# Kernel optimization log

Measured on AMD Instinct MI355X. Metric: run time of the kernel, lower is better.

Reference implementation:

```python
import jax, jax.numpy as jnp
import numpy as np

N, E, D, H, L = 50000, 800000, 64, 4, 2
DH = D // H


def layer_norm(h, g, b, eps=1e-5):
    mu = h.mean(-1, keepdims=True)
    var = ((h - mu) ** 2).mean(-1, keepdims=True)
    return (h - mu) / jnp.sqrt(var + eps) * g + b


def setup_inputs() -> dict:
    key = jax.random.key(0)
    ks = jax.random.split(key, 16)
    s = 1.0 / np.sqrt(D)
    inp = {
        "x": jax.random.normal(ks[0], (N, D), jnp.float32),
        "edge_attr": jax.random.normal(ks[1], (E, D), jnp.float32),
        "edge_index": jax.random.randint(ks[2], (2, E), 0, N, jnp.int64),
        "WQ": jax.random.normal(ks[3], (L, D, D), jnp.float32) * s,
        "WK": jax.random.normal(ks[4], (L, D, D), jnp.float32) * s,
        "WE": jax.random.normal(ks[5], (L, D, D), jnp.float32) * s,
        "WV": jax.random.normal(ks[6], (L, D, D), jnp.float32) * s,
        "WO": jax.random.normal(ks[7], (L, D, D), jnp.float32) * s,
        "bO": jnp.zeros((L, D), jnp.float32),
        "ln1_g": jnp.ones((L, D), jnp.float32),
        "ln1_b": jnp.zeros((L, D), jnp.float32),
        "W1": jax.random.normal(ks[8], (L, D, 2 * D), jnp.float32) * s,
        "b1": jnp.zeros((L, 2 * D), jnp.float32),
        "W2": jax.random.normal(ks[9], (L, 2 * D, D), jnp.float32) * (1.0 / np.sqrt(2 * D)),
        "b2": jnp.zeros((L, D), jnp.float32),
        "ln2_g": jnp.ones((L, D), jnp.float32),
        "ln2_b": jnp.zeros((L, D), jnp.float32),
    }
    return inp


def exphormer_layer(h, edge_attr, src, dst, p):
    (wq, wk, we, wv, wo, bo, g1, be1, w1, b1, w2, b2, g2, be2) = p
    n = h.shape[0]
    Qh = (h @ wq).reshape(n, H, DH)
    Kh = (h @ wk).reshape(n, H, DH)
    Vh = (h @ wv).reshape(n, H, DH)
    Eh = (edge_attr @ we).reshape(-1, H, DH)
    # per-edge score: sum over head_dim of K[src]*Q[dst]*E / sqrt(DH)
    s = jnp.sum(Kh[src] * Qh[dst] * Eh, axis=-1, keepdims=True) / np.sqrt(DH)
    score = jnp.exp(jnp.clip(s, -5.0, 5.0))  # [E, H, 1]
    msg = Vh[src] * score                     # [E, H, DH]
    wV = jax.ops.segment_sum(msg, dst, num_segments=n)    # [N, H, DH]
    Z = jax.ops.segment_sum(score, dst, num_segments=n)   # [N, H, 1]
    h_attn = (wV / (Z + 1e-6)).reshape(n, D)
    h1 = layer_norm(h + (h_attn @ wo + bo), g1, be1)
    ffn = jax.nn.relu(h1 @ w1 + b1) @ w2 + b2
    return layer_norm(h1 + ffn, g2, be2)


def reference(x, edge_attr, edge_index, WQ, WK, WE, WV, WO, bO, ln1_g, ln1_b,
              W1, b1, W2, b2, ln2_g, ln2_b):
    src = edge_index[0]
    dst = edge_index[1]
    h = x
    for l in range(L):
        p = (WQ[l], WK[l], WE[l], WV[l], WO[l], bO[l], ln1_g[l], ln1_b[l],
             W1[l], b1[l], W2[l], b2[l], ln2_g[l], ln2_b[l])
        h = exphormer_layer(h, edge_attr, src, dst, p)
    return h
```

## Files before the change

kernel.cpp:

```cpp
#include <hip/hip_runtime.h>

#define NN 50000
#define NE 800000
#define D  64
#define NL 2
#define NB 196

typedef __bf16 bf16x8 __attribute__((ext_vector_type(8)));
typedef float  floatx4 __attribute__((ext_vector_type(4)));

static __device__ __forceinline__ float bf2f(unsigned short u) {
    return __uint_as_float(((unsigned)u) << 16);
}
static __device__ __forceinline__ unsigned short f2bf(float x) {
    unsigned u = __float_as_uint(x);
    u += 0x7fff + ((u >> 16) & 1);
    return (unsigned short)(u >> 16);
}


__global__ void k_deg(const int* __restrict__ ei, int* __restrict__ deg) {
    int e = blockIdx.x * 256 + threadIdx.x;
    if (e < NE) atomicAdd(&deg[ei[NE + e]], 1);
}

__global__ __launch_bounds__(256) void k_scan1(const int* __restrict__ deg,
                                               int* __restrict__ psum) {
    __shared__ int red[4];
    int i = blockIdx.x * 256 + threadIdx.x;
    int v = (i < NN) ? deg[i] : 0;
#pragma unroll
    for (int m = 1; m < 64; m <<= 1) v += __shfl_xor(v, m, 64);
    if ((threadIdx.x & 63) == 0) red[threadIdx.x >> 6] = v;
    __syncthreads();
    if (threadIdx.x == 0) psum[blockIdx.x] = red[0] + red[1] + red[2] + red[3];
}

__global__ void k_scan2(int* __restrict__ psum) {
    __shared__ int buf[256];
    int t = threadIdx.x;
    int v = (t < NB) ? psum[t] : 0;
    buf[t] = v;
    __syncthreads();
    for (int o = 1; o < 256; o <<= 1) {
        int x = (t >= o) ? buf[t - o] : 0;
        __syncthreads();
        buf[t] += x;
        __syncthreads();
    }
    if (t < NB) psum[t] = buf[t] - v;
}

__global__ __launch_bounds__(256) void k_scan3(const int* __restrict__ deg,
                                               const int* __restrict__ psum,
                                               int* __restrict__ row_off,
                                               int* __restrict__ cursor) {
    __shared__ int buf[256];
    int t = threadIdx.x;
    int i = blockIdx.x * 256 + t;
    int v = (i < NN) ? deg[i] : 0;
    buf[t] = v;
    __syncthreads();
    for (int o = 1; o < 256; o <<= 1) {
        int x = (t >= o) ? buf[t - o] : 0;
        __syncthreads();
        buf[t] += x;
        __syncthreads();
    }
    if (i < NN) {
        int inc = buf[t] + psum[blockIdx.x];
        row_off[i + 1] = inc;
        cursor[i] = inc - v;
        if (i == 0) row_off[0] = 0;
    }
}

__global__ void k_scatter(const int* __restrict__ ei, int* __restrict__ cursor,
                          int* __restrict__ csr_src, int* __restrict__ eperm) {
    int e = blockIdx.x * 256 + threadIdx.x;
    if (e < NE) {
        int dst = ei[NE + e];
        int pos = atomicAdd(&cursor[dst], 1);
        csr_src[pos] = ei[e];
        eperm[e] = pos;
    }
}

__global__ __launch_bounds__(256) void k_prep(
        const float* __restrict__ WQ, const float* __restrict__ WK,
        const float* __restrict__ WV, const float* __restrict__ WE,
        const float* __restrict__ WO, const float* __restrict__ W1,
        const float* __restrict__ W2,
        unsigned short* __restrict__ wqT, unsigned short* __restrict__ wkT,
        unsigned short* __restrict__ wvT, unsigned short* __restrict__ weT,
        unsigned short* __restrict__ woT, unsigned short* __restrict__ w1T,
        unsigned short* __restrict__ w2T) {
    int idx = blockIdx.x * 256 + threadIdx.x;
    if (idx >= 2 * 36864) return;
    int l = idx / 36864;
    int r = idx % 36864;
    if (r < 20480) {
        int which = r >> 12, rr = r & 4095;
        int m = rr >> 6, k = rr & 63;
        const float* src = (which == 0 ? WQ : which == 1 ? WK : which == 2 ? WV :
                            which == 3 ? WE : WO);
        unsigned short* dst = (which == 0 ? wqT : which == 1 ? wkT : which == 2 ? wvT :
                               which == 3 ? weT : woT);
        dst[l * 4096 + rr] = f2bf(src[l * 4096 + k * 64 + m]);
    } else if (r < 28672) {
        int r2 = r - 20480;
        int m = r2 >> 6, k = r2 & 63;
        w1T[l * 8192 + r2] = f2bf(W1[l * 8192 + k * 128 + m]);
    } else {
        int r3 = r - 28672;
        int m = r3 >> 7, k = r3 & 127;
        w2T[l * 8192 + r3] = f2bf(W2[l * 8192 + k * 64 + m]);
    }
}


__global__ __launch_bounds__(256) void k_qkv_mfma(const float* __restrict__ h,
        const unsigned short* __restrict__ wqT, const unsigned short* __restrict__ wkT,
        const unsigned short* __restrict__ wvT,
        unsigned short* __restrict__ Qb, unsigned short* __restrict__ Kb,
        unsigned short* __restrict__ Vb) {
    __shared__ unsigned short st[4][16 * 72];
    const int lane = threadIdx.x & 63;
    const int w    = threadIdx.x >> 6;
    const int ml   = lane & 15;
    const int quad = lane >> 4;

    bf16x8 aq[2][4], ak[2][4], av[2][4];
#pragma unroll
    for (int kt = 0; kt < 2; kt++)
#pragma unroll
        for (int mt = 0; mt < 4; mt++) {
            int o = (mt*16 + ml)*64 + kt*32 + quad*8;
            aq[kt][mt] = *(const bf16x8*)&wqT[o];
            ak[kt][mt] = *(const bf16x8*)&wkT[o];
            av[kt][mt] = *(const bf16x8*)&wvT[o];
        }

    const int wave = blockIdx.x * 4 + w;
    const int nw   = gridDim.x * 4;
    const int el = lane >> 2, c = lane & 3;
    for (int tile = wave; tile < NN / 16; tile += nw) {
        const int e0 = tile * 16;
        const float4* ar = (const float4*)(h + (size_t)(e0 + ml) * D);
        bf16x8 b[2];
#pragma unroll
        for (int kt = 0; kt < 2; kt++) {
            float4 f0 = ar[kt*8 + quad*2 + 0];
            float4 f1 = ar[kt*8 + quad*2 + 1];
            b[kt][0] = (__bf16)f0.x; b[kt][1] = (__bf16)f0.y;
            b[kt][2] = (__bf16)f0.z; b[kt][3] = (__bf16)f0.w;
            b[kt][4] = (__bf16)f1.x; b[kt][5] = (__bf16)f1.y;
            b[kt][6] = (__bf16)f1.z; b[kt][7] = (__bf16)f1.w;
        }
        floatx4 accq[4] = {}, acck[4] = {}, accv[4] = {};
#pragma unroll
        for (int kt = 0; kt < 2; kt++)
#pragma unroll
            for (int mt = 0; mt < 4; mt++) {
                accq[mt] = __builtin_amdgcn_mfma_f32_16x16x32_bf16(aq[kt][mt], b[kt], accq[mt], 0, 0, 0);
                acck[mt] = __builtin_amdgcn_mfma_f32_16x16x32_bf16(ak[kt][mt], b[kt], acck[mt], 0, 0, 0);
                accv[mt] = __builtin_amdgcn_mfma_f32_16x16x32_bf16(av[kt][mt], b[kt], accv[mt], 0, 0, 0);
            }
#pragma unroll
        for (int mt = 0; mt < 4; mt++)
            *(ushort4*)&st[w][ml*72 + mt*16 + quad*4] =
                make_ushort4(f2bf(accq[mt][0]), f2bf(accq[mt][1]),
                             f2bf(accq[mt][2]), f2bf(accq[mt][3]));
        {
            uint4 r0 = *(const uint4*)&st[w][el*72 + c*16 + 0];
            uint4 r1 = *(const uint4*)&st[w][el*72 + c*16 + 8];
            uint4* gp = (uint4*)(Qb + (size_t)(e0 + el) * D + c*16);
            gp[0] = r0; gp[1] = r1;
        }
#pragma unroll
        for (int mt = 0; mt < 4; mt++)
            *(ushort4*)&st[w][ml*72 + mt*16 + quad*4] =
                make_ushort4(f2bf(acck[mt][0]), f2bf(acck[mt][1]),
                             f2bf(acck[mt][2]), f2bf(acck[mt][3]));
        {
            uint4 r0 = *(const uint4*)&st[w][el*72 + c*16 + 0];
            uint4 r1 = *(const uint4*)&st[w][el*72 + c*16 + 8];
            uint4* gp = (uint4*)(Kb + (size_t)(e0 + el) * D + c*16);
            gp[0] = r0; gp[1] = r1;
        }
#pragma unroll
        for (int mt = 0; mt < 4; mt++)
            *(ushort4*)&st[w][ml*72 + mt*16 + quad*4] =
                make_ushort4(f2bf(accv[mt][0]), f2bf(accv[mt][1]),
                             f2bf(accv[mt][2]), f2bf(accv[mt][3]));
        {
            uint4 r0 = *(const uint4*)&st[w][el*72 + c*16 + 0];
            uint4 r1 = *(const uint4*)&st[w][el*72 + c*16 + 8];
            uint4* gp = (uint4*)(Vb + (size_t)(e0 + el) * D + c*16);
            gp[0] = r0; gp[1] = r1;
        }
    }
}

__global__ __launch_bounds__(256) void k_eh_score(const float* __restrict__ ea,
        const unsigned short* __restrict__ weT, const int* __restrict__ eperm,
        const int* __restrict__ ei, const unsigned short* __restrict__ Qb,
        const unsigned short* __restrict__ Kb,
        float* __restrict__ scb, unsigned short* __restrict__ Eh1) {
    __shared__ unsigned short wsm[2 * 4608];
    __shared__ unsigned short st[4][16 * 72];
    const int t = threadIdx.x;
    for (int i = t; i < 1024; i += 256) {
        int l = i >> 9, r = i & 511;
        *(uint4*)&wsm[l*4608 + (r >> 3)*72 + (r & 7)*8] = ((const uint4*)weT)[i];
    }
    __syncthreads();

    const int lane = t & 63;
    const int w    = t >> 6;
    const int ml   = lane & 15;
    const int quad = lane >> 4;
    const int el = lane >> 2, c = lane & 3;
    const int wave = blockIdx.x * 4 + w;
    const int nw   = gridDim.x * 4;
    const int NT   = NE / 16;

    int tile = wave;
    if (tile >= NT) return;
    int srce = ei[tile*16 + el];
    int dste = ei[NE + tile*16 + el];
    int pose = eperm[tile*16 + el];
    const float4* ar0 = (const float4*)(ea + (size_t)(tile*16 + ml) * D);
    float4 f00 = ar0[quad*2 + 0];
    float4 f01 = ar0[quad*2 + 1];
    float4 f10 = ar0[8 + quad*2 + 0];
    float4 f11 = ar0[8 + quad*2 + 1];

    for (; tile < NT; tile += nw) {
        bf16x8 qg0 = *(const bf16x8*)(Qb + (size_t)dste * D + c*16);
        bf16x8 qg1 = *(const bf16x8*)(Qb + (size_t)dste * D + c*16 + 8);
        bf16x8 kg0 = *(const bf16x8*)(Kb + (size_t)srce * D + c*16);
        bf16x8 kg1 = *(const bf16x8*)(Kb + (size_t)srce * D + c*16 + 8);
        int nxt = tile + nw;
        float4 nf00 = f00, nf01 = f01, nf10 = f10, nf11 = f11;
        int nsrc = srce, ndst = dste, npos = pose;
        if (nxt < NT) {
            const float4* ar = (const float4*)(ea + (size_t)(nxt*16 + ml) * D);
            nf00 = ar[quad*2 + 0];
            nf01 = ar[quad*2 + 1];
            nf10 = ar[8 + quad*2 + 0];
            nf11 = ar[8 + quad*2 + 1];
            nsrc = ei[nxt*16 + el];
            ndst = ei[NE + nxt*16 + el];
            npos = eperm[nxt*16 + el];
        }
        bf16x8 b[2];
        b[0][0] = (__bf16)f00.x; b[0][1] = (__bf16)f00.y;
        b[0][2] = (__bf16)f00.z; b[0][3] = (__bf16)f00.w;
        b[0][4] = (__bf16)f01.x; b[0][5] = (__bf16)f01.y;
        b[0][6] = (__bf16)f01.z; b[0][7] = (__bf16)f01.w;
        b[1][0] = (__bf16)f10.x; b[1][1] = (__bf16)f10.y;
        b[1][2] = (__bf16)f10.z; b[1][3] = (__bf16)f10.w;
        b[1][4] = (__bf16)f11.x; b[1][5] = (__bf16)f11.y;
        b[1][6] = (__bf16)f11.z; b[1][7] = (__bf16)f11.w;

        {
            floatx4 acc[4] = {};
#pragma unroll
            for (int kt = 0; kt < 2; kt++)
#pragma unroll
                for (int mt = 0; mt < 4; mt++) {
                    bf16x8 a = *(const bf16x8*)&wsm[4608 + (mt*16 + ml)*72 + kt*32 + quad*8];
                    acc[mt] = __builtin_amdgcn_mfma_f32_16x16x32_bf16(a, b[kt], acc[mt], 0, 0, 0);
                }
#pragma unroll
            for (int mt = 0; mt < 4; mt++)
                *(ushort4*)&st[w][ml*72 + mt*16 + quad*4] =
                    make_ushort4(f2bf(acc[mt][0]), f2bf(acc[mt][1]),
                                 f2bf(acc[mt][2]), f2bf(acc[mt][3]));
            uint4 r0 = *(const uint4*)&st[w][el*72 + c*16 + 0];
            uint4 r1 = *(const uint4*)&st[w][el*72 + c*16 + 8];
            uint4* gp = (uint4*)(Eh1 + (size_t)(tile*16 + el) * D + c*16);
            gp[0] = r0;
            gp[1] = r1;
        }
        {
            floatx4 acc[4] = {};
#pragma unroll
            for (int kt = 0; kt < 2; kt++)
#pragma unroll
                for (int mt = 0; mt < 4; mt++) {
                    bf16x8 a = *(const bf16x8*)&wsm[(mt*16 + ml)*72 + kt*32 + quad*8];
                    acc[mt] = __builtin_amdgcn_mfma_f32_16x16x32_bf16(a, b[kt], acc[mt], 0, 0, 0);
                }
#pragma unroll
            for (int mt = 0; mt < 4; mt++)
                *(ushort4*)&st[w][ml*72 + mt*16 + quad*4] =
                    make_ushort4(f2bf(acc[mt][0]), f2bf(acc[mt][1]),
                                 f2bf(acc[mt][2]), f2bf(acc[mt][3]));
            bf16x8 e0v = *(const bf16x8*)&st[w][el*72 + c*16];
            bf16x8 e1v = *(const bf16x8*)&st[w][el*72 + c*16 + 8];
            float s = 0.f;
#pragma unroll
            for (int i = 0; i < 8; i++) s += (float)e0v[i] * (float)qg0[i] * (float)kg0[i];
#pragma unroll
            for (int i = 0; i < 8; i++) s += (float)e1v[i] * (float)qg1[i] * (float)kg1[i];
            scb[(size_t)pose * 4 + c] = __expf(fminf(5.f, fmaxf(-5.f, s * 0.25f)));
        }
        f00 = nf00; f01 = nf01; f10 = nf10; f11 = nf11;
        srce = nsrc; dste = ndst; pose = npos;
    }
}

__global__ __launch_bounds__(256) void k_score1(
        const unsigned short* __restrict__ Eh1,
        const unsigned short* __restrict__ Qb, const unsigned short* __restrict__ Kb,
        const int* __restrict__ ei, const int* __restrict__ eperm,
        float* __restrict__ scb) {
    const int lane = threadIdx.x & 63;
    const int w    = threadIdx.x >> 6;
    const int ml   = lane & 15;
    const int quad = lane >> 4;
    const int wave = blockIdx.x * 4 + w;
    const int nw   = gridDim.x * 4;
    const int NT   = NE / 16;
    int tile = wave;
    if (tile >= NT) return;
    int p0 = tile*16 + ml;
    int src = ei[p0], dst = ei[NE + p0], pos = eperm[p0];
    bf16x8 e0 = *(const bf16x8*)(Eh1 + (size_t)p0 * D + quad*16);
    bf16x8 e1 = *(const bf16x8*)(Eh1 + (size_t)p0 * D + quad*16 + 8);
    for (; tile < NT; tile += nw) {
        bf16x8 k0 = *(const bf16x8*)(Kb + (size_t)src * D + quad*16);
        bf16x8 k1 = *(const bf16x8*)(Kb + (size_t)src * D + quad*16 + 8);
        bf16x8 q0 = *(const bf16x8*)(Qb + (size_t)dst * D + quad*16);
        bf16x8 q1 = *(const bf16x8*)(Qb + (size_t)dst * D + quad*16 + 8);
        int nxt = tile + nw;
        int nsrc = src, ndst = dst, npos = pos;
        bf16x8 ne0 = e0, ne1 = e1;
        if (nxt < NT) {
            int pn = nxt*16 + ml;
            nsrc = ei[pn]; ndst = ei[NE + pn]; npos = eperm[pn];
            ne0 = *(const bf16x8*)(Eh1 + (size_t)pn * D + quad*16);
            ne1 = *(const bf16x8*)(Eh1 + (size_t)pn * D + quad*16 + 8);
        }
        float s = 0.f;
#pragma unroll
        for (int i = 0; i < 8; i++) s += (float)e0[i] * (float)q0[i] * (float)k0[i];
#pragma unroll
        for (int i = 0; i < 8; i++) s += (float)e1[i] * (float)q1[i] * (float)k1[i];
        scb[(size_t)pos * 4 + quad] = __expf(fminf(5.f, fmaxf(-5.f, s * 0.25f)));
        src = nsrc; dst = ndst; pos = npos; e0 = ne0; e1 = ne1;
    }
}

__global__ __launch_bounds__(256) void k_agg(
        const unsigned short* __restrict__ Vb, const float* __restrict__ scb,
        const int* __restrict__ row_off, const int* __restrict__ csr_src,
        unsigned short* __restrict__ h_attn) {
    const int node = blockIdx.x * 4 + (threadIdx.x >> 6);
    if (node >= NN) return;
    const int lane  = threadIdx.x & 63;
    const int eslot = lane >> 3;
    const int ml    = lane & 7;
    const int head  = ml >> 1;
    const int beg = row_off[node], end = row_off[node + 1];
    floatx4 a0 = {}, a1 = {};
    float z = 0.f;

    for (int cbeg = beg; cbeg < end; cbeg += 64) {
        const int cnt = min(64, end - cbeg);
        int myidx = cbeg + lane;
        int mysrc = (myidx < end) ? csr_src[myidx] : 0;

        for (int base = 0; base < cnt; base += 16) {
            int  jj[2];
            int  s[2];
            bool act[2];
#pragma unroll
            for (int u = 0; u < 2; u++) {
                int j = base + eslot + 8 * u;
                act[u] = j < cnt;
                jj[u]  = act[u] ? j : 0;
                s[u]   = __shfl(mysrc, jj[u], 64);
            }
            bf16x8 vb[2];
            float  sv[2];
#pragma unroll
            for (int u = 0; u < 2; u++) {
                vb[u] = *(const bf16x8*)(Vb + (size_t)s[u] * D + ml * 8);
                sv[u] = scb[(size_t)(cbeg + jj[u]) * 4 + head];
            }
#pragma unroll
            for (int u = 0; u < 2; u++) {
                float sc = act[u] ? sv[u] : 0.f;
                a0[0] += sc * (float)vb[u][0];
                a0[1] += sc * (float)vb[u][1];
                a0[2] += sc * (float)vb[u][2];
                a0[3] += sc * (float)vb[u][3];
                a1[0] += sc * (float)vb[u][4];
                a1[1] += sc * (float)vb[u][5];
                a1[2] += sc * (float)vb[u][6];
                a1[3] += sc * (float)vb[u][7];
                z += sc;
            }
        }
    }
#pragma unroll
    for (int m = 8; m <= 32; m <<= 1) {
#pragma unroll
        for (int r = 0; r < 4; r++) {
            a0[r] += __shfl_xor(a0[r], m, 64);
            a1[r] += __shfl_xor(a1[r], m, 64);
        }
        z += __shfl_xor(z, m, 64);
    }
    if (eslot == 0) {
        float inv = 1.f / (z + 1e-6f);
        unsigned r0 = ((unsigned)f2bf(a0[1] * inv) << 16) | f2bf(a0[0] * inv);
        unsigned r1 = ((unsigned)f2bf(a0[3] * inv) << 16) | f2bf(a0[2] * inv);
        unsigned r2 = ((unsigned)f2bf(a1[1] * inv) << 16) | f2bf(a1[0] * inv);
        unsigned r3 = ((unsigned)f2bf(a1[3] * inv) << 16) | f2bf(a1[2] * inv);
        *(uint4*)&h_attn[(size_t)node * D + ml * 8] = make_uint4(r0, r1, r2, r3);
    }
}

__global__ __launch_bounds__(512) void k_post_mfma(const float* __restrict__ h_in,
        const unsigned short* __restrict__ h_attn,
        const unsigned short* __restrict__ woT_g,
        const unsigned short* __restrict__ w1T_g,
        const unsigned short* __restrict__ w2T_g,
        const float* __restrict__ bo,
        const float* __restrict__ g1, const float* __restrict__ be1,
        const float* __restrict__ b1, const float* __restrict__ b2,
        const float* __restrict__ g2, const float* __restrict__ be2,
        float* __restrict__ h_out) {
    __shared__ unsigned short woT_s[64 * 72];
    __shared__ unsigned short w1T_s[128 * 72];
    __shared__ unsigned short w2T_s[64 * 136];
    __shared__ unsigned short stg[8][16 * 136];

    const int t = threadIdx.x;
    {
        const uint4* s0 = (const uint4*)woT_g;
        { int i = t; if (i < 512) { int row = i >> 3, c = i & 7;
              *(uint4*)&woT_s[row*72 + c*8] = s0[i]; } }
        const uint4* s1 = (const uint4*)w1T_g;
        for (int i = t; i < 1024; i += 512) {
            int row = i >> 3, c = i & 7;
            *(uint4*)&w1T_s[row*72 + c*8] = s1[i];
        }
        const uint4* s2 = (const uint4*)w2T_g;
        for (int i = t; i < 1024; i += 512) {
            int row = i >> 4, c = i & 15;
            *(uint4*)&w2T_s[row*136 + c*8] = s2[i];
        }
    }
    __syncthreads();

    const int w = t >> 6, lane = t & 63;
    const int ml = lane & 15, quad = lane >> 4;
    const int tile = blockIdx.x * 8 + w;
    if (tile >= NN / 16) return;
    const int e0 = tile * 16;
    unsigned short* st = stg[w];

    floatx4 acc1[4] = {};
#pragma unroll
    for (int kt = 0; kt < 2; kt++) {
        bf16x8 b = *(const bf16x8*)(h_attn + (size_t)(e0 + ml) * D + kt*32 + quad*8);
#pragma unroll
        for (int mt = 0; mt < 4; mt++) {
            bf16x8 a = *(const bf16x8*)&woT_s[(mt*16 + ml)*72 + kt*32 + quad*8];
            acc1[mt] = __builtin_amdgcn_mfma_f32_16x16x32_bf16(a, b, acc1[mt], 0, 0, 0);
        }
    }
    const float4* hp  = (const float4*)(h_in + (size_t)(e0 + ml) * D);
    const float4* bo4 = (const float4*)bo;
    floatx4 tt[4];
#pragma unroll
    for (int mt = 0; mt < 4; mt++) {
        float4 hh = hp[mt*4 + quad];
        float4 bb = bo4[mt*4 + quad];
        tt[mt][0] = acc1[mt][0] + hh.x + bb.x;
        tt[mt][1] = acc1[mt][1] + hh.y + bb.y;
        tt[mt][2] = acc1[mt][2] + hh.z + bb.z;
        tt[mt][3] = acc1[mt][3] + hh.w + bb.w;
    }
    float s = 0.f;
#pragma unroll
    for (int mt = 0; mt < 4; mt++) s += tt[mt][0] + tt[mt][1] + tt[mt][2] + tt[mt][3];
    s += __shfl_xor(s, 16, 64); s += __shfl_xor(s, 32, 64);
    float mu = s * (1.f / 64.f);
    float v = 0.f;
#pragma unroll
    for (int mt = 0; mt < 4; mt++)
#pragma unroll
        for (int r = 0; r < 4; r++) { float c = tt[mt][r] - mu; v += c * c; }
    v += __shfl_xor(v, 16, 64); v += __shfl_xor(v, 32, 64);
    float rstd = rsqrtf(v * (1.f / 64.f) + 1e-5f);
    const float4* g1v  = (const float4*)g1;
    const float4* be1v = (const float4*)be1;
    floatx4 h1[4];
#pragma unroll
    for (int mt = 0; mt < 4; mt++) {
        float4 gg = g1v[mt*4 + quad];
        float4 bb = be1v[mt*4 + quad];
        h1[mt][0] = (tt[mt][0] - mu) * rstd * gg.x + bb.x;
        h1[mt][1] = (tt[mt][1] - mu) * rstd * gg.y + bb.y;
        h1[mt][2] = (tt[mt][2] - mu) * rstd * gg.z + bb.z;
        h1[mt][3] = (tt[mt][3] - mu) * rstd * gg.w + bb.w;
        *(ushort4*)&st[ml*136 + mt*16 + quad*4] =
            make_ushort4(f2bf(h1[mt][0]), f2bf(h1[mt][1]), f2bf(h1[mt][2]), f2bf(h1[mt][3]));
    }

    bf16x8 bh[2];
#pragma unroll
    for (int kt = 0; kt < 2; kt++)
        bh[kt] = *(const bf16x8*)&st[ml*136 + kt*32 + quad*8];
    floatx4 acc2[8] = {};
#pragma unroll
    for (int kt = 0; kt < 2; kt++)
#pragma unroll
        for (int mt = 0; mt < 8; mt++) {
            bf16x8 a = *(const bf16x8*)&w1T_s[(mt*16 + ml)*72 + kt*32 + quad*8];
            acc2[mt] = __builtin_amdgcn_mfma_f32_16x16x32_bf16(a, bh[kt], acc2[mt], 0, 0, 0);
        }
    const float4* b1v = (const float4*)b1;
#pragma unroll
    for (int mt = 0; mt < 8; mt++) {
        float4 bb = b1v[mt*4 + quad];
        float y0 = fmaxf(acc2[mt][0] + bb.x, 0.f);
        float y1 = fmaxf(acc2[mt][1] + bb.y, 0.f);
        float y2 = fmaxf(acc2[mt][2] + bb.z, 0.f);
        float y3 = fmaxf(acc2[mt][3] + bb.w, 0.f);
        *(ushort4*)&st[ml*136 + mt*16 + quad*4] =
            make_ushort4(f2bf(y0), f2bf(y1), f2bf(y2), f2bf(y3));
    }

    floatx4 acc3[4] = {};
#pragma unroll
    for (int kt = 0; kt < 4; kt++) {
        bf16x8 b = *(const bf16x8*)&st[ml*136 + kt*32 + quad*8];
#pragma unroll
        for (int mt = 0; mt < 4; mt++) {
            bf16x8 a = *(const bf16x8*)&w2T_s[(mt*16 + ml)*136 + kt*32 + quad*8];
            acc3[mt] = __builtin_amdgcn_mfma_f32_16x16x32_bf16(a, b, acc3[mt], 0, 0, 0);
        }
    }
    const float4* b2v = (const float4*)b2;
#pragma unroll
    for (int mt = 0; mt < 4; mt++) {
        float4 bb = b2v[mt*4 + quad];
        tt[mt][0] = acc3[mt][0] + bb.x + h1[mt][0];
        tt[mt][1] = acc3[mt][1] + bb.y + h1[mt][1];
        tt[mt][2] = acc3[mt][2] + bb.z + h1[mt][2];
        tt[mt][3] = acc3[mt][3] + bb.w + h1[mt][3];
    }
    s = 0.f;
#pragma unroll
    for (int mt = 0; mt < 4; mt++) s += tt[mt][0] + tt[mt][1] + tt[mt][2] + tt[mt][3];
    s += __shfl_xor(s, 16, 64); s += __shfl_xor(s, 32, 64);
    mu = s * (1.f / 64.f);
    v = 0.f;
#pragma unroll
    for (int mt = 0; mt < 4; mt++)
#pragma unroll
        for (int r = 0; r < 4; r++) { float c = tt[mt][r] - mu; v += c * c; }
    v += __shfl_xor(v, 16, 64); v += __shfl_xor(v, 32, 64);
    rstd = rsqrtf(v * (1.f / 64.f) + 1e-5f);
    const float4* g2v  = (const float4*)g2;
    const float4* be2v = (const float4*)be2;
    float4* outp = (float4*)(h_out + (size_t)(e0 + ml) * D);
#pragma unroll
    for (int mt = 0; mt < 4; mt++) {
        float4 gg = g2v[mt*4 + quad];
        float4 bb = be2v[mt*4 + quad];
        float4 o;
        o.x = (tt[mt][0] - mu) * rstd * gg.x + bb.x;
        o.y = (tt[mt][1] - mu) * rstd * gg.y + bb.y;
        o.z = (tt[mt][2] - mu) * rstd * gg.z + bb.z;
        o.w = (tt[mt][3] - mu) * rstd * gg.w + bb.w;
        outp[mt*4 + quad] = o;
    }
}


extern "C" void kernel_launch(void* const* d_in, const int* in_sizes, int n_in,
                              void* d_out, int out_size, void* d_ws, size_t ws_size,
                              hipStream_t stream) {
    const float* x   = (const float*)d_in[0];
    const float* ea  = (const float*)d_in[1];
    const int*   ei  = (const int*)d_in[2];
    const float* WQ  = (const float*)d_in[3];
    const float* WK  = (const float*)d_in[4];
    const float* WE  = (const float*)d_in[5];
    const float* WV  = (const float*)d_in[6];
    const float* WO  = (const float*)d_in[7];
    const float* bO  = (const float*)d_in[8];
    const float* g1  = (const float*)d_in[9];
    const float* be1 = (const float*)d_in[10];
    const float* W1  = (const float*)d_in[11];
    const float* b1  = (const float*)d_in[12];
    const float* W2  = (const float*)d_in[13];
    const float* b2  = (const float*)d_in[14];
    const float* g2  = (const float*)d_in[15];
    const float* be2 = (const float*)d_in[16];
    float* out = (float*)d_out;

    char* wsb = (char*)d_ws;
    size_t off = 0;
    auto alloc = [&](size_t bytes) {
        void* p = wsb + off;
        off += (bytes + 255) & ~(size_t)255;
        return p;
    };
    unsigned short* Qb   = (unsigned short*)alloc((size_t)NN * D * 2);
    unsigned short* Kb   = (unsigned short*)alloc((size_t)NN * D * 2);
    unsigned short* Vb   = (unsigned short*)alloc((size_t)NN * D * 2);
    float* hbuf          = (float*)alloc((size_t)NN * D * 4);
    unsigned short* hattn= (unsigned short*)alloc((size_t)NN * D * 2);
    unsigned short* Eh1  = (unsigned short*)alloc((size_t)NE * D * 2);
    float* scb           = (float*)alloc((size_t)NE * 4 * 4);
    int* row_off         = (int*)alloc((size_t)(NN + 1) * 4);
    int* cursor          = (int*)alloc((size_t)NN * 4);
    int* deg             = (int*)alloc((size_t)NN * 4);
    int* psum            = (int*)alloc((size_t)256 * 4);
    int* csr_src         = (int*)alloc((size_t)NE * 4);
    int* eperm           = (int*)alloc((size_t)NE * 4);
    unsigned short* wqT  = (unsigned short*)alloc((size_t)2 * 4096 * 2);
    unsigned short* wkT  = (unsigned short*)alloc((size_t)2 * 4096 * 2);
    unsigned short* wvT  = (unsigned short*)alloc((size_t)2 * 4096 * 2);
    unsigned short* weT  = (unsigned short*)alloc((size_t)2 * 4096 * 2);
    unsigned short* woT  = (unsigned short*)alloc((size_t)2 * 4096 * 2);
    unsigned short* w1T  = (unsigned short*)alloc((size_t)2 * 8192 * 2);
    unsigned short* w2T  = (unsigned short*)alloc((size_t)2 * 8192 * 2);

    hipMemsetAsync(deg, 0, (size_t)NN * 4, stream);
    k_deg<<<(NE + 255) / 256, 256, 0, stream>>>(ei, deg);
    k_scan1<<<NB, 256, 0, stream>>>(deg, psum);
    k_scan2<<<1, 256, 0, stream>>>(psum);
    k_scan3<<<NB, 256, 0, stream>>>(deg, psum, row_off, cursor);
    k_scatter<<<(NE + 255) / 256, 256, 0, stream>>>(ei, cursor, csr_src, eperm);
    k_prep<<<(2 * 36864 + 255) / 256, 256, 0, stream>>>(WQ, WK, WV, WE, WO, W1, W2,
            wqT, wkT, wvT, weT, woT, w1T, w2T);

    k_qkv_mfma<<<782, 256, 0, stream>>>(x, wqT, wkT, wvT, Qb, Kb, Vb);
    k_eh_score<<<1280, 256, 0, stream>>>(ea, weT, eperm, ei, Qb, Kb, scb, Eh1);

    k_agg<<<(NN + 3) / 4, 256, 0, stream>>>(Vb, scb, row_off, csr_src, hattn);
    k_post_mfma<<<(NN / 16 + 7) / 8, 512, 0, stream>>>(x, hattn,
            woT, w1T, w2T, bO, g1, be1, b1, b2, g2, be2, hbuf);

    k_qkv_mfma<<<782, 256, 0, stream>>>(hbuf, wqT + 4096, wkT + 4096,
                                        wvT + 4096, Qb, Kb, Vb);
    k_score1<<<1536, 256, 0, stream>>>(Eh1, Qb, Kb, ei, eperm, scb);
    k_agg<<<(NN + 3) / 4, 256, 0, stream>>>(Vb, scb, row_off, csr_src, hattn);
    k_post_mfma<<<(NN / 16 + 7) / 8, 512, 0, stream>>>(hbuf, hattn,
            woT + 4096, w1T + 8192, w2T + 8192,
            bO + 64, g1 + 64, be1 + 64, b1 + 128, b2 + 64,
            g2 + 64, be2 + 64, out);
}
```

Measured before the change: 614.2 us.

## Process edges in CSR order and compute scores directly from MFMA accumulators

```diff
diff --git a/kernel.cpp b/kernel.cpp
--- a/kernel.cpp
+++ b/kernel.cpp
@@ -76,13 +76,15 @@
 }
 
 __global__ void k_scatter(const int* __restrict__ ei, int* __restrict__ cursor,
-                          int* __restrict__ csr_src, int* __restrict__ eperm) {
+                          int* __restrict__ csr_src, int* __restrict__ csr_dst,
+                          int* __restrict__ csr_eid) {
     int e = blockIdx.x * 256 + threadIdx.x;
     if (e < NE) {
         int dst = ei[NE + e];
         int pos = atomicAdd(&cursor[dst], 1);
         csr_src[pos] = ei[e];
-        eperm[e] = pos;
+        csr_dst[pos] = dst;
+        csr_eid[pos] = e;
     }
 }
 
@@ -203,12 +205,12 @@
 }
 
 __global__ __launch_bounds__(256) void k_eh_score(const float* __restrict__ ea,
-        const unsigned short* __restrict__ weT, const int* __restrict__ eperm,
-        const int* __restrict__ ei, const unsigned short* __restrict__ Qb,
-        const unsigned short* __restrict__ Kb,
+        const unsigned short* __restrict__ weT,
+        const int* __restrict__ csr_eid, const int* __restrict__ csr_src,
+        const int* __restrict__ csr_dst,
+        const unsigned short* __restrict__ Qb, const unsigned short* __restrict__ Kb,
         float* __restrict__ scb, unsigned short* __restrict__ Eh1) {
     __shared__ unsigned short wsm[2 * 4608];
-    __shared__ unsigned short st[4][16 * 72];
     const int t = threadIdx.x;
     for (int i = t; i < 1024; i += 256) {
         int l = i >> 9, r = i & 511;
@@ -220,39 +222,49 @@
     const int w    = t >> 6;
     const int ml   = lane & 15;
     const int quad = lane >> 4;
-    const int el = lane >> 2, c = lane & 3;
     const int wave = blockIdx.x * 4 + w;
     const int nw   = gridDim.x * 4;
     const int NT   = NE / 16;
 
     int tile = wave;
     if (tile >= NT) return;
-    int srce = ei[tile*16 + el];
-    int dste = ei[NE + tile*16 + el];
-    int pose = eperm[tile*16 + el];
-    const float4* ar0 = (const float4*)(ea + (size_t)(tile*16 + ml) * D);
+    int src0 = csr_src[tile*16 + ml];
+    int dst0 = csr_dst[tile*16 + ml];
+    int eid0 = csr_eid[tile*16 + ml];
+    const float4* ar0 = (const float4*)(ea + (size_t)eid0 * D);
     float4 f00 = ar0[quad*2 + 0];
     float4 f01 = ar0[quad*2 + 1];
     float4 f10 = ar0[8 + quad*2 + 0];
     float4 f11 = ar0[8 + quad*2 + 1];
+    int nxt1 = tile + nw;
+    int eid1 = eid0, src1 = src0, dst1 = dst0;
+    if (nxt1 < NT) {
+        eid1 = csr_eid[nxt1*16 + ml];
+        src1 = csr_src[nxt1*16 + ml];
+        dst1 = csr_dst[nxt1*16 + ml];
+    }
 
     for (; tile < NT; tile += nw) {
-        bf16x8 qg0 = *(const bf16x8*)(Qb + (size_t)dste * D + c*16);
-        bf16x8 qg1 = *(const bf16x8*)(Qb + (size_t)dste * D + c*16 + 8);
-        bf16x8 kg0 = *(const bf16x8*)(Kb + (size_t)srce * D + c*16);
-        bf16x8 kg1 = *(const bf16x8*)(Kb + (size_t)srce * D + c*16 + 8);
-        int nxt = tile + nw;
         float4 nf00 = f00, nf01 = f01, nf10 = f10, nf11 = f11;
-        int nsrc = srce, ndst = dste, npos = pose;
-        if (nxt < NT) {
-            const float4* ar = (const float4*)(ea + (size_t)(nxt*16 + ml) * D);
+        if (tile + nw < NT) {
+            const float4* ar = (const float4*)(ea + (size_t)eid1 * D);
             nf00 = ar[quad*2 + 0];
             nf01 = ar[quad*2 + 1];
             nf10 = ar[8 + quad*2 + 0];
             nf11 = ar[8 + quad*2 + 1];
-            nsrc = ei[nxt*16 + el];
-            ndst = ei[NE + nxt*16 + el];
-            npos = eperm[nxt*16 + el];
+        }
+        ushort4 qg[4], kg[4];
+#pragma unroll
+        for (int mt = 0; mt < 4; mt++) {
+            qg[mt] = *(const ushort4*)(Qb + (size_t)dst0 * D + mt*16 + quad*4);
+            kg[mt] = *(const ushort4*)(Kb + (size_t)src0 * D + mt*16 + quad*4);
+        }
+        int nxt2 = tile + 2*nw;
+        int eid2 = eid1, src2 = src1, dst2 = dst1;
+        if (nxt2 < NT) {
+            eid2 = csr_eid[nxt2*16 + ml];
+            src2 = csr_src[nxt2*16 + ml];
+            dst2 = csr_dst[nxt2*16 + ml];
         }
         bf16x8 b[2];
         b[0][0] = (__bf16)f00.x; b[0][1] = (__bf16)f00.y;
@@ -273,16 +285,12 @@
                     bf16x8 a = *(const bf16x8*)&wsm[4608 + (mt*16 + ml)*72 + kt*32 + quad*8];
                     acc[mt] = __builtin_amdgcn_mfma_f32_16x16x32_bf16(a, b[kt], acc[mt], 0, 0, 0);
                 }
+            unsigned short* base = Eh1 + (size_t)(tile*16 + ml) * D;
 #pragma unroll
             for (int mt = 0; mt < 4; mt++)
-                *(ushort4*)&st[w][ml*72 + mt*16 + quad*4] =
+                *(ushort4*)(base + mt*16 + quad*4) =
                     make_ushort4(f2bf(acc[mt][0]), f2bf(acc[mt][1]),
                                  f2bf(acc[mt][2]), f2bf(acc[mt][3]));
-            uint4 r0 = *(const uint4*)&st[w][el*72 + c*16 + 0];
-            uint4 r1 = *(const uint4*)&st[w][el*72 + c*16 + 8];
-            uint4* gp = (uint4*)(Eh1 + (size_t)(tile*16 + el) * D + c*16);
-            gp[0] = r0;
-            gp[1] = r1;
         }
         {
             floatx4 acc[4] = {};
@@ -293,29 +301,31 @@
                     bf16x8 a = *(const bf16x8*)&wsm[(mt*16 + ml)*72 + kt*32 + quad*8];
                     acc[mt] = __builtin_amdgcn_mfma_f32_16x16x32_bf16(a, b[kt], acc[mt], 0, 0, 0);
                 }
-#pragma unroll
-            for (int mt = 0; mt < 4; mt++)
-                *(ushort4*)&st[w][ml*72 + mt*16 + quad*4] =
-                    make_ushort4(f2bf(acc[mt][0]), f2bf(acc[mt][1]),
-                                 f2bf(acc[mt][2]), f2bf(acc[mt][3]));
-            bf16x8 e0v = *(const bf16x8*)&st[w][el*72 + c*16];
-            bf16x8 e1v = *(const bf16x8*)&st[w][el*72 + c*16 + 8];
-            float s = 0.f;
-#pragma unroll
-            for (int i = 0; i < 8; i++) s += (float)e0v[i] * (float)qg0[i] * (float)kg0[i];
-#pragma unroll
-            for (int i = 0; i < 8; i++) s += (float)e1v[i] * (float)qg1[i] * (float)kg1[i];
-            scb[(size_t)pose * 4 + c] = __expf(fminf(5.f, fmaxf(-5.f, s * 0.25f)));
+            float scq[4];
+#pragma unroll
+            for (int mt = 0; mt < 4; mt++) {
+                float p = acc[mt][0] * bf2f(qg[mt].x) * bf2f(kg[mt].x)
+                        + acc[mt][1] * bf2f(qg[mt].y) * bf2f(kg[mt].y)
+                        + acc[mt][2] * bf2f(qg[mt].z) * bf2f(kg[mt].z)
+                        + acc[mt][3] * bf2f(qg[mt].w) * bf2f(kg[mt].w);
+                p += __shfl_xor(p, 16, 64);
+                p += __shfl_xor(p, 32, 64);
+                scq[mt] = __expf(fminf(5.f, fmaxf(-5.f, p * 0.25f)));
+            }
+            if (quad == 0)
+                *(float4*)(scb + (size_t)(tile*16 + ml) * 4) =
+                    make_float4(scq[0], scq[1], scq[2], scq[3]);
         }
         f00 = nf00; f01 = nf01; f10 = nf10; f11 = nf11;
-        srce = nsrc; dste = ndst; pose = npos;
+        src0 = src1; dst0 = dst1;
+        eid1 = eid2; src1 = src2; dst1 = dst2;
     }
 }
 
 __global__ __launch_bounds__(256) void k_score1(
         const unsigned short* __restrict__ Eh1,
         const unsigned short* __restrict__ Qb, const unsigned short* __restrict__ Kb,
-        const int* __restrict__ ei, const int* __restrict__ eperm,
+        const int* __restrict__ csr_src, const int* __restrict__ csr_dst,
         float* __restrict__ scb) {
     const int lane = threadIdx.x & 63;
     const int w    = threadIdx.x >> 6;
@@ -327,7 +337,7 @@
     int tile = wave;
     if (tile >= NT) return;
     int p0 = tile*16 + ml;
-    int src = ei[p0], dst = ei[NE + p0], pos = eperm[p0];
+    int src = csr_src[p0], dst = csr_dst[p0];
     bf16x8 e0 = *(const bf16x8*)(Eh1 + (size_t)p0 * D + quad*16);
     bf16x8 e1 = *(const bf16x8*)(Eh1 + (size_t)p0 * D + quad*16 + 8);
     for (; tile < NT; tile += nw) {
@@ -336,11 +346,11 @@
         bf16x8 q0 = *(const bf16x8*)(Qb + (size_t)dst * D + quad*16);
         bf16x8 q1 = *(const bf16x8*)(Qb + (size_t)dst * D + quad*16 + 8);
         int nxt = tile + nw;
-        int nsrc = src, ndst = dst, npos = pos;
+        int nsrc = src, ndst = dst;
         bf16x8 ne0 = e0, ne1 = e1;
         if (nxt < NT) {
             int pn = nxt*16 + ml;
-            nsrc = ei[pn]; ndst = ei[NE + pn]; npos = eperm[pn];
+            nsrc = csr_src[pn]; ndst = csr_dst[pn];
             ne0 = *(const bf16x8*)(Eh1 + (size_t)pn * D + quad*16);
             ne1 = *(const bf16x8*)(Eh1 + (size_t)pn * D + quad*16 + 8);
         }
@@ -349,8 +359,8 @@
         for (int i = 0; i < 8; i++) s += (float)e0[i] * (float)q0[i] * (float)k0[i];
 #pragma unroll
         for (int i = 0; i < 8; i++) s += (float)e1[i] * (float)q1[i] * (float)k1[i];
-        scb[(size_t)pos * 4 + quad] = __expf(fminf(5.f, fmaxf(-5.f, s * 0.25f)));
-        src = nsrc; dst = ndst; pos = npos; e0 = ne0; e1 = ne1;
+        scb[(size_t)(tile*16 + ml) * 4 + quad] = __expf(fminf(5.f, fmaxf(-5.f, s * 0.25f)));
+        src = nsrc; dst = ndst; e0 = ne0; e1 = ne1;
     }
 }
 
@@ -627,7 +637,8 @@
     int* deg             = (int*)alloc((size_t)NN * 4);
     int* psum            = (int*)alloc((size_t)256 * 4);
     int* csr_src         = (int*)alloc((size_t)NE * 4);
-    int* eperm           = (int*)alloc((size_t)NE * 4);
+    int* csr_dst         = (int*)alloc((size_t)NE * 4);
+    int* csr_eid         = (int*)alloc((size_t)NE * 4);
     unsigned short* wqT  = (unsigned short*)alloc((size_t)2 * 4096 * 2);
     unsigned short* wkT  = (unsigned short*)alloc((size_t)2 * 4096 * 2);
     unsigned short* wvT  = (unsigned short*)alloc((size_t)2 * 4096 * 2);
@@ -641,12 +652,13 @@
     k_scan1<<<NB, 256, 0, stream>>>(deg, psum);
     k_scan2<<<1, 256, 0, stream>>>(psum);
     k_scan3<<<NB, 256, 0, stream>>>(deg, psum, row_off, cursor);
-    k_scatter<<<(NE + 255) / 256, 256, 0, stream>>>(ei, cursor, csr_src, eperm);
+    k_scatter<<<(NE + 255) / 256, 256, 0, stream>>>(ei, cursor, csr_src, csr_dst, csr_eid);
     k_prep<<<(2 * 36864 + 255) / 256, 256, 0, stream>>>(WQ, WK, WV, WE, WO, W1, W2,
             wqT, wkT, wvT, weT, woT, w1T, w2T);
 
     k_qkv_mfma<<<782, 256, 0, stream>>>(x, wqT, wkT, wvT, Qb, Kb, Vb);
-    k_eh_score<<<1280, 256, 0, stream>>>(ea, weT, eperm, ei, Qb, Kb, scb, Eh1);
+    k_eh_score<<<1536, 256, 0, stream>>>(ea, weT, csr_eid, csr_src, csr_dst,
+                                         Qb, Kb, scb, Eh1);
 
     k_agg<<<(NN + 3) / 4, 256, 0, stream>>>(Vb, scb, row_off, csr_src, hattn);
     k_post_mfma<<<(NN / 16 + 7) / 8, 512, 0, stream>>>(x, hattn,
@@ -654,7 +666,7 @@
 
     k_qkv_mfma<<<782, 256, 0, stream>>>(hbuf, wqT + 4096, wkT + 4096,
                                         wvT + 4096, Qb, Kb, Vb);
-    k_score1<<<1536, 256, 0, stream>>>(Eh1, Qb, Kb, ei, eperm, scb);
+    k_score1<<<1536, 256, 0, stream>>>(Eh1, Qb, Kb, csr_src, csr_dst, scb);
     k_agg<<<(NN + 3) / 4, 256, 0, stream>>>(Vb, scb, row_off, csr_src, hattn);
     k_post_mfma<<<(NN / 16 + 7) / 8, 512, 0, stream>>>(hbuf, hattn,
             woT + 4096, w1T + 8192, w2T + 8192,
```

Result: no change. 609.4 us (-0.8%).
